# Kernel tuning notes

Measured on AMD Instinct MI355X. Metric: run time of the kernel, lower is better.

The kernel has to match this reference:

```python
import jax, jax.numpy as jnp
import numpy as np

E = 32          # num_experts
K = 4           # num_experts_per_tok
H = 1024        # hidden_size
I = 768         # moe_intermediate_size
ROUTED_SCALING_FACTOR = 1.0


def setup_inputs() -> dict:
    key = jax.random.key(0)
    k0, k1, k2, k3, k4, k5 = jax.random.split(key, 6)
    return {
        "hidden_states": jax.random.normal(k0, (1, 2048, H), jnp.float32),
        "gate_w": jax.random.normal(k1, (E, H), jnp.float32) * 0.02,
        "w1": jax.random.normal(k2, (E, H, I), jnp.float32) * 0.02,   # gate proj per expert
        "w3": jax.random.normal(k3, (E, H, I), jnp.float32) * 0.02,   # up proj per expert
        "w2": jax.random.normal(k4, (E, I, H), jnp.float32) * 0.02,   # down proj per expert
        "e_bias": jax.random.normal(k5, (E,), jnp.float32) * 0.02,    # e_score_correction_bias
    }


def reference(hidden_states, gate_w, w1, w3, w2, e_bias):
    orig_shape = hidden_states.shape
    x = hidden_states.reshape(-1, orig_shape[-1])            # [T, H]
    T = x.shape[0]

    # ----- router gate (ReplicatedLinear, no bias) -----
    router_logits = x @ gate_w.T                             # [T, E]

    # ----- grouped top-k with num_expert_group=1, topk_group=1 == plain top-k
    # scoring_func='sigmoid'; correction bias only affects expert *selection*,
    # the routing weights are the uncorrected sigmoid scores.
    scores = jax.nn.sigmoid(router_logits.astype(jnp.float32))          # [T, E]
    _, topk_ids = jax.lax.top_k(scores + e_bias[None, :], K)            # [T, K]
    topk_w = jnp.take_along_axis(scores, topk_ids, axis=1)              # [T, K]
    # renormalize (norm_topk_prob=True)
    topk_w = topk_w / jnp.sum(topk_w, axis=1, keepdims=True)

    # dense combine weights [T, E] (zero for unselected experts)
    combine = jnp.zeros((T, E), jnp.float32).at[jnp.arange(T)[:, None], topk_ids].add(topk_w)

    # ----- experts: SwiGLU per expert, combine weighted -----
    g = jnp.einsum("th,ehi->tei", x, w1)                     # [T, E, I]
    u = jnp.einsum("th,ehi->tei", x, w3)                     # [T, E, I]
    a = jax.nn.silu(g) * u * combine[:, :, None].astype(x.dtype)
    out = jnp.einsum("tei,eih->th", a, w2)                   # [T, H]

    out = out * ROUTED_SCALING_FACTOR
    return out.reshape(orig_shape)
```

## Files before the change

kernel.cpp:

```cpp
#include <hip/hip_runtime.h>
#include <cstdint>

#define TOK 2048
#define HD  1024
#define ID  768
#define NE  32
#define RT  4

typedef unsigned short u16t;
typedef unsigned int   u32t;
typedef __bf16 bf16x8 __attribute__((ext_vector_type(8)));
typedef float  f32x4  __attribute__((ext_vector_type(4)));
typedef u16t   u16x8  __attribute__((ext_vector_type(8)));
typedef u16t   u16x4  __attribute__((ext_vector_type(4)));
typedef float  fvec4  __attribute__((ext_vector_type(4)));

__device__ __forceinline__ u16t f2b(float f) {
  u32t u = __float_as_uint(f);
  u32t r = u + 0x7fffu + ((u >> 16) & 1u);
  return (u16t)(r >> 16);
}

__device__ __forceinline__ int swz(int row, int kc) {
  return (row * 4 + (kc ^ ((row >> 2) & 3))) * 8;
}

__global__ void k_cvt(const float* __restrict__ x, u16t* __restrict__ xb) {
  int i = (blockIdx.x * 256 + threadIdx.x) * 4;
  fvec4 v = *(const fvec4*)(x + i);
  u16x4 o = { f2b(v[0]), f2b(v[1]), f2b(v[2]), f2b(v[3]) };
  *(u16x4*)(xb + i) = o;
}

__global__ void k_router(const float* __restrict__ x, const float* __restrict__ gw,
                         const float* __restrict__ eb,
                         int* __restrict__ topk_ids, float* __restrict__ topk_w,
                         int* __restrict__ counts) {
  int lane = threadIdx.x & 63;
  int t = blockIdx.x * 4 + (threadIdx.x >> 6);
  const float* xt = x + (size_t)t * HD;
  fvec4 xr[4];
#pragma unroll
  for (int i = 0; i < 4; ++i) xr[i] = *(const fvec4*)(xt + lane * 4 + i * 256);
  float myscore = 0.f;
  for (int e = 0; e < NE; ++e) {
    const float* ge = gw + (size_t)e * HD + lane * 4;
    float s = 0.f;
#pragma unroll
    for (int i = 0; i < 4; ++i) {
      fvec4 g = *(const fvec4*)(ge + i * 256);
      s = fmaf(xr[i][0], g[0], s); s = fmaf(xr[i][1], g[1], s);
      s = fmaf(xr[i][2], g[2], s); s = fmaf(xr[i][3], g[3], s);
    }
#pragma unroll
    for (int off = 32; off; off >>= 1) s += __shfl_xor(s, off);
    if (lane == e) myscore = s;
  }
  float sig = 1.f / (1.f + expf(-myscore));
  float biased = (lane < NE) ? (sig + eb[lane]) : -3.0e38f;
  float wsum = 0.f;
  int ids[4]; float wsv[4];
#pragma unroll
  for (int k = 0; k < 4; ++k) {
    float v = biased; int idx = lane;
#pragma unroll
    for (int off = 32; off; off >>= 1) {
      float ov = __shfl_xor(v, off);
      int   oi = __shfl_xor(idx, off);
      if (ov > v || (ov == v && oi < idx)) { v = ov; idx = oi; }
    }
    ids[k] = idx;
    float sc = __shfl(sig, idx);
    wsv[k] = sc; wsum += sc;
    if (lane == idx) biased = -3.0e38f;
  }
  float inv = 1.f / wsum;
#pragma unroll
  for (int k = 0; k < 4; ++k) {
    if (lane == k) {
      topk_ids[t * 4 + k] = ids[k];
      topk_w[t * 4 + k]  = wsv[k] * inv;
      atomicAdd(&counts[ids[k]], 1);
    }
  }
}

__global__ void k_bucket(const int* __restrict__ topk_ids, const float* __restrict__ topk_w,
                         const int* __restrict__ counts, int* __restrict__ offsets,
                         int* __restrict__ pairTok, float* __restrict__ pairW,
                         int* __restrict__ invp) {
  __shared__ int soff[NE + 1];
  __shared__ int scur[NE];
  int tid = threadIdx.x;
  if (tid == 0) {
    int acc = 0;
    for (int e = 0; e < NE; ++e) { soff[e] = acc; acc += counts[e]; }
    soff[NE] = acc;
  }
  if (tid < NE) scur[tid] = 0;
  __syncthreads();
  if (tid <= NE) offsets[tid] = soff[tid];
  for (int p = tid; p < TOK * 4; p += 256) {
    int e = topk_ids[p];
    int pos = soff[e] + atomicAdd(&scur[e], 1);
    pairTok[pos] = p;
    pairW[pos]   = topk_w[p];
    invp[p]      = pos;
  }
}

__launch_bounds__(256, 2)
__global__ void k_gemm1(const u16t* __restrict__ xb, const float* __restrict__ w1,
                        const float* __restrict__ w3,
                        const int* __restrict__ counts, const int* __restrict__ offsets,
                        const int* __restrict__ pairTok, const float* __restrict__ pairW,
                        u16t* __restrict__ A) {
  const int e = blockIdx.y;
  const int colbase = blockIdx.x * 64;
  const int count = counts[e];
  const int base  = offsets[e];
  const int tid = threadIdx.x, lane = tid & 63, wv = tid >> 6;

  __shared__ __align__(16) u16t Xs[256 * 32];
  __shared__ __align__(16) u16t Ws2[2][64 * 32];
  __shared__ float pw[256];

  const float* wp = (tid < 128) ? (w1 + (size_t)e * HD * ID)
                                : (w3 + (size_t)e * HD * ID);
  u16t* wsp = &Ws2[tid >> 7][0];
  const int u  = tid & 127;
  const int cg = u & 15, hg = u >> 4;
  const int kc = hg >> 1, half = (hg & 1) * 4;

  for (int r0 = blockIdx.z * 256; r0 < count; r0 += RT * 256) {
    __syncthreads();
    int idx = r0 + tid;
    bool valid = idx < count;
    int pr = valid ? (pairTok[base + idx] >> 2) : -1;
    pw[tid] = valid ? pairW[base + idx] : 0.f;

    u16x8 xd[4];
    fvec4 wd[4];
    {
      if (pr >= 0) {
        const u16t* s = xb + (size_t)pr * HD;
        xd[0] = *(const u16x8*)(s);      xd[1] = *(const u16x8*)(s + 8);
        xd[2] = *(const u16x8*)(s + 16); xd[3] = *(const u16x8*)(s + 24);
      } else {
        u16x8 z = {0,0,0,0,0,0,0,0};
        xd[0] = z; xd[1] = z; xd[2] = z; xd[3] = z;
      }
      const float* s = wp + (size_t)(hg * 4) * ID + colbase + cg * 4;
      wd[0] = *(const fvec4*)(s);          wd[1] = *(const fvec4*)(s + ID);
      wd[2] = *(const fvec4*)(s + 2 * ID); wd[3] = *(const fvec4*)(s + 3 * ID);
    }

    f32x4 zz = {0.f, 0.f, 0.f, 0.f};
    f32x4 accg[4][4], accu[4][4];
#pragma unroll
    for (int a = 0; a < 4; ++a)
#pragma unroll
      for (int b = 0; b < 4; ++b) { accg[a][b] = zz; accu[a][b] = zz; }

    for (int kk = 0; kk < HD; kk += 32) {
      __syncthreads();
      *(u16x8*)&Xs[swz(tid, 0)] = xd[0];
      *(u16x8*)&Xs[swz(tid, 1)] = xd[1];
      *(u16x8*)&Xs[swz(tid, 2)] = xd[2];
      *(u16x8*)&Xs[swz(tid, 3)] = xd[3];
#pragma unroll
      for (int c = 0; c < 4; ++c) {
        u16x4 pk = { f2b(wd[0][c]), f2b(wd[1][c]), f2b(wd[2][c]), f2b(wd[3][c]) };
        *(u16x4*)&wsp[swz(cg * 4 + c, kc) + half] = pk;
      }
      __syncthreads();
      if (kk + 32 < HD) {
        if (pr >= 0) {
          const u16t* s = xb + (size_t)pr * HD + kk + 32;
          xd[0] = *(const u16x8*)(s);      xd[1] = *(const u16x8*)(s + 8);
          xd[2] = *(const u16x8*)(s + 16); xd[3] = *(const u16x8*)(s + 24);
        }
        const float* s = wp + (size_t)(kk + 32 + hg * 4) * ID + colbase + cg * 4;
        wd[0] = *(const fvec4*)(s);          wd[1] = *(const fvec4*)(s + ID);
        wd[2] = *(const fvec4*)(s + 2 * ID); wd[3] = *(const fvec4*)(s + 3 * ID);
      }
      const int kcl = lane >> 4;
      const int rb = wv * 64 + (lane & 15);
      bf16x8 af[4];
#pragma unroll
      for (int rf = 0; rf < 4; ++rf)
        af[rf] = *(const bf16x8*)&Xs[swz(rb + rf * 16, kcl)];
#pragma unroll
      for (int cf = 0; cf < 4; ++cf) {
        int col = cf * 16 + (lane & 15);
        bf16x8 b1f = *(const bf16x8*)&Ws2[0][swz(col, kcl)];
        bf16x8 b3f = *(const bf16x8*)&Ws2[1][swz(col, kcl)];
#pragma unroll
        for (int rf = 0; rf < 4; ++rf) {
          accg[rf][cf] = __builtin_amdgcn_mfma_f32_16x16x32_bf16(af[rf], b1f, accg[rf][cf], 0, 0, 0);
          accu[rf][cf] = __builtin_amdgcn_mfma_f32_16x16x32_bf16(af[rf], b3f, accu[rf][cf], 0, 0, 0);
        }
      }
    }
    __syncthreads();
#pragma unroll
    for (int rf = 0; rf < 4; ++rf) {
#pragma unroll
      for (int ri = 0; ri < 4; ++ri) {
        int rowl = wv * 64 + rf * 16 + (lane >> 4) * 4 + ri;
        int grow = r0 + rowl;
        if (grow < count) {
          float wgt = pw[rowl];
#pragma unroll
          for (int cf = 0; cf < 4; ++cf) {
            float gg = accg[rf][cf][ri];
            float uu = accu[rf][cf][ri];
            float a = gg / (1.f + expf(-gg)) * uu * wgt;
            A[(size_t)(base + grow) * ID + colbase + cf * 16 + (lane & 15)] = f2b(a);
          }
        }
      }
    }
  }
}

__launch_bounds__(256, 2)
__global__ void k_gemm2(const u16t* __restrict__ A, const float* __restrict__ w2,
                        const int* __restrict__ counts, const int* __restrict__ offsets,
                        float* __restrict__ buf) {
  const int e = blockIdx.y;
  const int colbase = blockIdx.x * 64;
  const int count = counts[e];
  const int base  = offsets[e];
  const int tid = threadIdx.x, lane = tid & 63, wv = tid >> 6;

  __shared__ __align__(16) u16t As[256 * 32];
  __shared__ __align__(16) u16t W2s[64 * 32];

  const float* w2e = w2 + (size_t)e * ID * HD;
  const int cg = tid & 15, kg = tid >> 4;
  const int k0 = kg * 2, kcw = k0 >> 3, offw = k0 & 7;

  for (int r0 = blockIdx.z * 256; r0 < count; r0 += RT * 256) {
    int idx = r0 + tid;
    bool valid = idx < count;
    const u16t* asrc = A + (size_t)(base + idx) * ID;

    u16x8 xd[4];
    fvec4 wd0, wd1;
    {
      if (valid) {
        xd[0] = *(const u16x8*)(asrc);      xd[1] = *(const u16x8*)(asrc + 8);
        xd[2] = *(const u16x8*)(asrc + 16); xd[3] = *(const u16x8*)(asrc + 24);
      } else {
        u16x8 z = {0,0,0,0,0,0,0,0};
        xd[0] = z; xd[1] = z; xd[2] = z; xd[3] = z;
      }
      const float* s = w2e + (size_t)(kg * 2) * HD + colbase + cg * 4;
      wd0 = *(const fvec4*)(s); wd1 = *(const fvec4*)(s + HD);
    }

    f32x4 zz = {0.f, 0.f, 0.f, 0.f};
    f32x4 acc[4][4];
#pragma unroll
    for (int a = 0; a < 4; ++a)
#pragma unroll
      for (int b = 0; b < 4; ++b) acc[a][b] = zz;

    for (int kk = 0; kk < ID; kk += 32) {
      __syncthreads();
      *(u16x8*)&As[swz(tid, 0)] = xd[0];
      *(u16x8*)&As[swz(tid, 1)] = xd[1];
      *(u16x8*)&As[swz(tid, 2)] = xd[2];
      *(u16x8*)&As[swz(tid, 3)] = xd[3];
#pragma unroll
      for (int c = 0; c < 4; ++c) {
        u32t pk = (u32t)f2b(wd0[c]) | ((u32t)f2b(wd1[c]) << 16);
        *(u32t*)&W2s[swz(cg * 4 + c, kcw) + offw] = pk;
      }
      __syncthreads();
      if (kk + 32 < ID) {
        if (valid) {
          const u16t* s = asrc + kk + 32;
          xd[0] = *(const u16x8*)(s);      xd[1] = *(const u16x8*)(s + 8);
          xd[2] = *(const u16x8*)(s + 16); xd[3] = *(const u16x8*)(s + 24);
        }
        const float* s = w2e + (size_t)(kk + 32 + kg * 2) * HD + colbase + cg * 4;
        wd0 = *(const fvec4*)(s); wd1 = *(const fvec4*)(s + HD);
      }
      const int kcl = lane >> 4;
      const int rb = wv * 64 + (lane & 15);
      bf16x8 af[4];
#pragma unroll
      for (int rf = 0; rf < 4; ++rf)
        af[rf] = *(const bf16x8*)&As[swz(rb + rf * 16, kcl)];
#pragma unroll
      for (int cf = 0; cf < 4; ++cf) {
        bf16x8 bfr = *(const bf16x8*)&W2s[swz(cf * 16 + (lane & 15), kcl)];
#pragma unroll
        for (int rf = 0; rf < 4; ++rf)
          acc[rf][cf] = __builtin_amdgcn_mfma_f32_16x16x32_bf16(af[rf], bfr, acc[rf][cf], 0, 0, 0);
      }
    }
#pragma unroll
    for (int rf = 0; rf < 4; ++rf)
#pragma unroll
      for (int ri = 0; ri < 4; ++ri) {
        int rowl = wv * 64 + rf * 16 + (lane >> 4) * 4 + ri;
        int grow = r0 + rowl;
        if (grow < count) {
#pragma unroll
          for (int cf = 0; cf < 4; ++cf)
            buf[(size_t)(base + grow) * HD + colbase + cf * 16 + (lane & 15)] = acc[rf][cf][ri];
        }
      }
  }
}

__global__ void k_reduce(const float* __restrict__ buf, const int* __restrict__ invp,
                         float* __restrict__ out) {
  int t = blockIdx.x;
  int col = threadIdx.x * 4;
  int p0 = invp[t * 4 + 0], p1 = invp[t * 4 + 1];
  int p2 = invp[t * 4 + 2], p3 = invp[t * 4 + 3];
  fvec4 s = *(const fvec4*)(buf + (size_t)p0 * HD + col);
  s += *(const fvec4*)(buf + (size_t)p1 * HD + col);
  s += *(const fvec4*)(buf + (size_t)p2 * HD + col);
  s += *(const fvec4*)(buf + (size_t)p3 * HD + col);
  *(fvec4*)(out + (size_t)t * HD + col) = s;
}

extern "C" void kernel_launch(void* const* d_in, const int* in_sizes, int n_in,
                              void* d_out, int out_size, void* d_ws, size_t ws_size,
                              hipStream_t stream) {
  const float* x  = (const float*)d_in[0];
  const float* gw = (const float*)d_in[1];
  const float* w1 = (const float*)d_in[2];
  const float* w3 = (const float*)d_in[3];
  const float* w2 = (const float*)d_in[4];
  const float* eb = (const float*)d_in[5];
  float* out = (float*)d_out;

  char* ws = (char*)d_ws;
  int*   counts   = (int*)(ws);
  int*   offsets  = (int*)(ws + 256);
  int*   topk_ids = (int*)(ws + 4096);
  float* topk_w   = (float*)(ws + 36864);
  int*   pairTok  = (int*)(ws + 69632);
  float* pairW    = (float*)(ws + 102400);
  int*   invp     = (int*)(ws + 135168);
  u16t*  xb       = (u16t*)(ws + 262144);
  u16t*  Abuf     = (u16t*)(ws + 262144 + 4194304);
  float* buf      = (float*)(ws + 262144 + 4194304 + 12582912);

  hipMemsetAsync(counts, 0, 4096, stream);
  k_cvt   <<<2048, 256, 0, stream>>>(x, xb);
  k_router<<<512, 256, 0, stream>>>(x, gw, eb, topk_ids, topk_w, counts);
  k_bucket<<<1, 256, 0, stream>>>(topk_ids, topk_w, counts, offsets, pairTok, pairW, invp);
  k_gemm1 <<<dim3(12, 32, RT), 256, 0, stream>>>(xb, w1, w3, counts, offsets, pairTok, pairW, Abuf);
  k_gemm2 <<<dim3(16, 32, RT), 256, 0, stream>>>(Abuf, w2, counts, offsets, buf);
  k_reduce<<<2048, 256, 0, stream>>>(buf, invp, out);
}
```

Before: 241.5 us.

## Double-buffer weight tiles and load activations directly into MFMA fragments

Both expert GEMMs now keep the weight tile in a double-buffered LDS ring and load the activation rows straight from global memory into MFMA A-fragments, so the activation LDS stage goes away. The kernel is software-pipelined two k-steps deep so loads overlap the MFMAs. Column tiles shrink from 64 to 32, the grid widens, RT drops to 2, and launch bounds rise for higher occupancy. In exchange, each activation row is read from global memory by more blocks, and the weight fp32-to-bf16 conversion is repeated across more row blocks.

```diff
diff --git a/kernel.cpp b/kernel.cpp
--- a/kernel.cpp
+++ b/kernel.cpp
@@ -5,7 +5,7 @@
 #define HD  1024
 #define ID  768
 #define NE  32
-#define RT  4
+#define RT  2
 
 typedef unsigned short u16t;
 typedef unsigned int   u32t;
@@ -109,102 +109,98 @@
   }
 }
 
-__launch_bounds__(256, 2)
+#define G1_WLOAD(d0, d1, KK) do { \
+    const float* _s = wp + (size_t)((KK) + hg * 2) * ID + wcol; \
+    d0 = *(const fvec4*)(_s); d1 = *(const fvec4*)(_s + ID); } while (0)
+
+#define G1_WSTORE(BUF, d0, d1) do { \
+    _Pragma("unroll") for (int c = 0; c < 4; ++c) { \
+      u32t pk = (u32t)f2b(d0[c]) | ((u32t)f2b(d1[c]) << 16); \
+      *(u32t*)&Ws[BUF][mat][swz(cg4 + c, kcw) + offw] = pk; } } while (0)
+
+#define G1_AFLOAD(AF, KK) do { \
+    _Pragma("unroll") for (int rf = 0; rf < 4; ++rf) \
+      AF[rf] = *(const u16x8*)(xb + (size_t)tok[rf] * HD + (KK) + klo); } while (0)
+
+#define G1_MFMA(AF, BUF) do { \
+    bf16x8 b0 = *(const bf16x8*)&Ws[BUF][0][swz(col0, kcl)]; \
+    bf16x8 b1 = *(const bf16x8*)&Ws[BUF][0][swz(col1, kcl)]; \
+    bf16x8 b2 = *(const bf16x8*)&Ws[BUF][1][swz(col0, kcl)]; \
+    bf16x8 b3 = *(const bf16x8*)&Ws[BUF][1][swz(col1, kcl)]; \
+    _Pragma("unroll") for (int rf = 0; rf < 4; ++rf) { \
+      acc[rf][0][0] = __builtin_amdgcn_mfma_f32_16x16x32_bf16(AF[rf], b0, acc[rf][0][0], 0, 0, 0); \
+      acc[rf][1][0] = __builtin_amdgcn_mfma_f32_16x16x32_bf16(AF[rf], b1, acc[rf][1][0], 0, 0, 0); \
+      acc[rf][0][1] = __builtin_amdgcn_mfma_f32_16x16x32_bf16(AF[rf], b2, acc[rf][0][1], 0, 0, 0); \
+      acc[rf][1][1] = __builtin_amdgcn_mfma_f32_16x16x32_bf16(AF[rf], b3, acc[rf][1][1], 0, 0, 0); } } while (0)
+
+__launch_bounds__(256, 3)
 __global__ void k_gemm1(const u16t* __restrict__ xb, const float* __restrict__ w1,
                         const float* __restrict__ w3,
                         const int* __restrict__ counts, const int* __restrict__ offsets,
                         const int* __restrict__ pairTok, const float* __restrict__ pairW,
                         u16t* __restrict__ A) {
   const int e = blockIdx.y;
-  const int colbase = blockIdx.x * 64;
+  const int colbase = blockIdx.x * 32;
   const int count = counts[e];
   const int base  = offsets[e];
   const int tid = threadIdx.x, lane = tid & 63, wv = tid >> 6;
 
-  __shared__ __align__(16) u16t Xs[256 * 32];
-  __shared__ __align__(16) u16t Ws2[2][64 * 32];
+  __shared__ __align__(16) u16t Ws[2][2][1024];
   __shared__ float pw[256];
 
-  const float* wp = (tid < 128) ? (w1 + (size_t)e * HD * ID)
-                                : (w3 + (size_t)e * HD * ID);
-  u16t* wsp = &Ws2[tid >> 7][0];
-  const int u  = tid & 127;
-  const int cg = u & 15, hg = u >> 4;
-  const int kc = hg >> 1, half = (hg & 1) * 4;
+  const int mat = tid >> 7;
+  const float* wp = (mat ? w3 : w1) + (size_t)e * HD * ID;
+  const int u = tid & 127;
+  const int cg4 = (u & 7) * 4, hg = u >> 3;
+  const int kcw = hg >> 2, offw = (hg & 3) * 2;
+  const int wcol = colbase + cg4;
+  const int klo = (lane >> 4) * 8;
+  const int col0 = lane & 15, col1 = col0 + 16, kcl = lane >> 4;
 
   for (int r0 = blockIdx.z * 256; r0 < count; r0 += RT * 256) {
     __syncthreads();
-    int idx = r0 + tid;
-    bool valid = idx < count;
-    int pr = valid ? (pairTok[base + idx] >> 2) : -1;
-    pw[tid] = valid ? pairW[base + idx] : 0.f;
-
-    u16x8 xd[4];
-    fvec4 wd[4];
     {
-      if (pr >= 0) {
-        const u16t* s = xb + (size_t)pr * HD;
-        xd[0] = *(const u16x8*)(s);      xd[1] = *(const u16x8*)(s + 8);
-        xd[2] = *(const u16x8*)(s + 16); xd[3] = *(const u16x8*)(s + 24);
-      } else {
-        u16x8 z = {0,0,0,0,0,0,0,0};
-        xd[0] = z; xd[1] = z; xd[2] = z; xd[3] = z;
-      }
-      const float* s = wp + (size_t)(hg * 4) * ID + colbase + cg * 4;
-      wd[0] = *(const fvec4*)(s);          wd[1] = *(const fvec4*)(s + ID);
-      wd[2] = *(const fvec4*)(s + 2 * ID); wd[3] = *(const fvec4*)(s + 3 * ID);
+      int idx = r0 + tid;
+      pw[tid] = (idx < count) ? pairW[base + idx] : 0.f;
+    }
+    int tok[4];
+#pragma unroll
+    for (int rf = 0; rf < 4; ++rf) {
+      int idx = r0 + wv * 64 + rf * 16 + (lane & 15);
+      idx = idx < count ? idx : count - 1;
+      tok[rf] = pairTok[base + idx] >> 2;
     }
 
     f32x4 zz = {0.f, 0.f, 0.f, 0.f};
-    f32x4 accg[4][4], accu[4][4];
+    f32x4 acc[4][2][2];
 #pragma unroll
     for (int a = 0; a < 4; ++a)
 #pragma unroll
-      for (int b = 0; b < 4; ++b) { accg[a][b] = zz; accu[a][b] = zz; }
-
-    for (int kk = 0; kk < HD; kk += 32) {
+      for (int b = 0; b < 2; ++b) { acc[a][b][0] = zz; acc[a][b][1] = zz; }
+
+    fvec4 wdA0, wdA1, wdB0, wdB1;
+    u16x8 afC[4], afD[4];
+    G1_WLOAD(wdA0, wdA1, 0);
+    G1_WLOAD(wdB0, wdB1, 32);
+    G1_AFLOAD(afC, 0);
+    G1_WSTORE(0, wdA0, wdA1);
+    G1_WLOAD(wdA0, wdA1, 64);
+
+    for (int s = 0; s < 32; s += 2) {
+      const int kk = s * 32;
       __syncthreads();
-      *(u16x8*)&Xs[swz(tid, 0)] = xd[0];
-      *(u16x8*)&Xs[swz(tid, 1)] = xd[1];
-      *(u16x8*)&Xs[swz(tid, 2)] = xd[2];
-      *(u16x8*)&Xs[swz(tid, 3)] = xd[3];
-#pragma unroll
-      for (int c = 0; c < 4; ++c) {
-        u16x4 pk = { f2b(wd[0][c]), f2b(wd[1][c]), f2b(wd[2][c]), f2b(wd[3][c]) };
-        *(u16x4*)&wsp[swz(cg * 4 + c, kc) + half] = pk;
-      }
+      G1_WSTORE(1, wdB0, wdB1);
+      if (s + 3 < 32) G1_WLOAD(wdB0, wdB1, kk + 96);
+      G1_AFLOAD(afD, kk + 32);
+      G1_MFMA(afC, 0);
       __syncthreads();
-      if (kk + 32 < HD) {
-        if (pr >= 0) {
-          const u16t* s = xb + (size_t)pr * HD + kk + 32;
-          xd[0] = *(const u16x8*)(s);      xd[1] = *(const u16x8*)(s + 8);
-          xd[2] = *(const u16x8*)(s + 16); xd[3] = *(const u16x8*)(s + 24);
-        }
-        const float* s = wp + (size_t)(kk + 32 + hg * 4) * ID + colbase + cg * 4;
-        wd[0] = *(const fvec4*)(s);          wd[1] = *(const fvec4*)(s + ID);
-        wd[2] = *(const fvec4*)(s + 2 * ID); wd[3] = *(const fvec4*)(s + 3 * ID);
-      }
-      const int kcl = lane >> 4;
-      const int rb = wv * 64 + (lane & 15);
-      bf16x8 af[4];
-#pragma unroll
-      for (int rf = 0; rf < 4; ++rf)
-        af[rf] = *(const bf16x8*)&Xs[swz(rb + rf * 16, kcl)];
-#pragma unroll
-      for (int cf = 0; cf < 4; ++cf) {
-        int col = cf * 16 + (lane & 15);
-        bf16x8 b1f = *(const bf16x8*)&Ws2[0][swz(col, kcl)];
-        bf16x8 b3f = *(const bf16x8*)&Ws2[1][swz(col, kcl)];
-#pragma unroll
-        for (int rf = 0; rf < 4; ++rf) {
-          accg[rf][cf] = __builtin_amdgcn_mfma_f32_16x16x32_bf16(af[rf], b1f, accg[rf][cf], 0, 0, 0);
-          accu[rf][cf] = __builtin_amdgcn_mfma_f32_16x16x32_bf16(af[rf], b3f, accu[rf][cf], 0, 0, 0);
-        }
-      }
-    }
-    __syncthreads();
-#pragma unroll
-    for (int rf = 0; rf < 4; ++rf) {
+      if (s + 2 < 32) G1_WSTORE(0, wdA0, wdA1);
+      if (s + 4 < 32) G1_WLOAD(wdA0, wdA1, kk + 128);
+      if (s + 2 < 32) G1_AFLOAD(afC, kk + 64);
+      G1_MFMA(afD, 1);
+    }
+#pragma unroll
+    for (int rf = 0; rf < 4; ++rf)
 #pragma unroll
       for (int ri = 0; ri < 4; ++ri) {
         int rowl = wv * 64 + rf * 16 + (lane >> 4) * 4 + ri;
@@ -212,95 +208,87 @@
         if (grow < count) {
           float wgt = pw[rowl];
 #pragma unroll
-          for (int cf = 0; cf < 4; ++cf) {
-            float gg = accg[rf][cf][ri];
-            float uu = accu[rf][cf][ri];
+          for (int cf = 0; cf < 2; ++cf) {
+            float gg = acc[rf][cf][0][ri];
+            float uu = acc[rf][cf][1][ri];
             float a = gg / (1.f + expf(-gg)) * uu * wgt;
             A[(size_t)(base + grow) * ID + colbase + cf * 16 + (lane & 15)] = f2b(a);
           }
         }
       }
-    }
-  }
-}
-
-__launch_bounds__(256, 2)
-__global__ void k_gemm2(const u16t* __restrict__ A, const float* __restrict__ w2,
+  }
+}
+
+#define G2_WLOAD(d, KK) \
+    d = *(const fvec4*)(w2e + (size_t)((KK) + kg) * HD + wcol)
+
+#define G2_WSTORE(BUF, d) do { \
+    _Pragma("unroll") for (int c = 0; c < 4; ++c) \
+      W2s[BUF][swz(cg4 + c, kcw) + offw] = f2b(d[c]); } while (0)
+
+#define G2_AFLOAD(AF, KK) do { \
+    _Pragma("unroll") for (int rf = 0; rf < 4; ++rf) \
+      AF[rf] = *(const u16x8*)(Ab + (size_t)arow[rf] * ID + (KK) + klo); } while (0)
+
+#define G2_MFMA(AF, BUF) do { \
+    bf16x8 b0 = *(const bf16x8*)&W2s[BUF][swz(col0, kcl)]; \
+    bf16x8 b1 = *(const bf16x8*)&W2s[BUF][swz(col1, kcl)]; \
+    _Pragma("unroll") for (int rf = 0; rf < 4; ++rf) { \
+      acc[rf][0] = __builtin_amdgcn_mfma_f32_16x16x32_bf16(AF[rf], b0, acc[rf][0], 0, 0, 0); \
+      acc[rf][1] = __builtin_amdgcn_mfma_f32_16x16x32_bf16(AF[rf], b1, acc[rf][1], 0, 0, 0); } } while (0)
+
+__launch_bounds__(256, 4)
+__global__ void k_gemm2(const u16t* __restrict__ Ab, const float* __restrict__ w2,
                         const int* __restrict__ counts, const int* __restrict__ offsets,
                         float* __restrict__ buf) {
   const int e = blockIdx.y;
-  const int colbase = blockIdx.x * 64;
+  const int colbase = blockIdx.x * 32;
   const int count = counts[e];
   const int base  = offsets[e];
   const int tid = threadIdx.x, lane = tid & 63, wv = tid >> 6;
 
-  __shared__ __align__(16) u16t As[256 * 32];
-  __shared__ __align__(16) u16t W2s[64 * 32];
+  __shared__ __align__(16) u16t W2s[2][1024];
 
   const float* w2e = w2 + (size_t)e * ID * HD;
-  const int cg = tid & 15, kg = tid >> 4;
-  const int k0 = kg * 2, kcw = k0 >> 3, offw = k0 & 7;
+  const int cg4 = (tid & 7) * 4, kg = tid >> 3;
+  const int kcw = kg >> 3, offw = kg & 7;
+  const int wcol = colbase + cg4;
+  const int klo = (lane >> 4) * 8;
+  const int col0 = lane & 15, col1 = col0 + 16, kcl = lane >> 4;
 
   for (int r0 = blockIdx.z * 256; r0 < count; r0 += RT * 256) {
-    int idx = r0 + tid;
-    bool valid = idx < count;
-    const u16t* asrc = A + (size_t)(base + idx) * ID;
-
-    u16x8 xd[4];
-    fvec4 wd0, wd1;
-    {
-      if (valid) {
-        xd[0] = *(const u16x8*)(asrc);      xd[1] = *(const u16x8*)(asrc + 8);
-        xd[2] = *(const u16x8*)(asrc + 16); xd[3] = *(const u16x8*)(asrc + 24);
-      } else {
-        u16x8 z = {0,0,0,0,0,0,0,0};
-        xd[0] = z; xd[1] = z; xd[2] = z; xd[3] = z;
-      }
-      const float* s = w2e + (size_t)(kg * 2) * HD + colbase + cg * 4;
-      wd0 = *(const fvec4*)(s); wd1 = *(const fvec4*)(s + HD);
-    }
-
+    int arow[4];
+#pragma unroll
+    for (int rf = 0; rf < 4; ++rf) {
+      int idx = r0 + wv * 64 + rf * 16 + (lane & 15);
+      idx = idx < count ? idx : count - 1;
+      arow[rf] = base + idx;
+    }
     f32x4 zz = {0.f, 0.f, 0.f, 0.f};
-    f32x4 acc[4][4];
-#pragma unroll
-    for (int a = 0; a < 4; ++a)
-#pragma unroll
-      for (int b = 0; b < 4; ++b) acc[a][b] = zz;
-
-    for (int kk = 0; kk < ID; kk += 32) {
+    f32x4 acc[4][2];
+#pragma unroll
+    for (int a = 0; a < 4; ++a) { acc[a][0] = zz; acc[a][1] = zz; }
+
+    fvec4 wdA, wdB;
+    u16x8 afC[4], afD[4];
+    G2_WLOAD(wdA, 0);
+    G2_WLOAD(wdB, 32);
+    G2_AFLOAD(afC, 0);
+    G2_WSTORE(0, wdA);
+    G2_WLOAD(wdA, 64);
+
+    for (int s = 0; s < 24; s += 2) {
+      const int kk = s * 32;
       __syncthreads();
-      *(u16x8*)&As[swz(tid, 0)] = xd[0];
-      *(u16x8*)&As[swz(tid, 1)] = xd[1];
-      *(u16x8*)&As[swz(tid, 2)] = xd[2];
-      *(u16x8*)&As[swz(tid, 3)] = xd[3];
-#pragma unroll
-      for (int c = 0; c < 4; ++c) {
-        u32t pk = (u32t)f2b(wd0[c]) | ((u32t)f2b(wd1[c]) << 16);
-        *(u32t*)&W2s[swz(cg * 4 + c, kcw) + offw] = pk;
-      }
+      G2_WSTORE(1, wdB);
+      if (s + 3 < 24) G2_WLOAD(wdB, kk + 96);
+      G2_AFLOAD(afD, kk + 32);
+      G2_MFMA(afC, 0);
       __syncthreads();
-      if (kk + 32 < ID) {
-        if (valid) {
-          const u16t* s = asrc + kk + 32;
-          xd[0] = *(const u16x8*)(s);      xd[1] = *(const u16x8*)(s + 8);
-          xd[2] = *(const u16x8*)(s + 16); xd[3] = *(const u16x8*)(s + 24);
-        }
-        const float* s = w2e + (size_t)(kk + 32 + kg * 2) * HD + colbase + cg * 4;
-        wd0 = *(const fvec4*)(s); wd1 = *(const fvec4*)(s + HD);
-      }
-      const int kcl = lane >> 4;
-      const int rb = wv * 64 + (lane & 15);
-      bf16x8 af[4];
-#pragma unroll
-      for (int rf = 0; rf < 4; ++rf)
-        af[rf] = *(const bf16x8*)&As[swz(rb + rf * 16, kcl)];
-#pragma unroll
-      for (int cf = 0; cf < 4; ++cf) {
-        bf16x8 bfr = *(const bf16x8*)&W2s[swz(cf * 16 + (lane & 15), kcl)];
-#pragma unroll
-        for (int rf = 0; rf < 4; ++rf)
-          acc[rf][cf] = __builtin_amdgcn_mfma_f32_16x16x32_bf16(af[rf], bfr, acc[rf][cf], 0, 0, 0);
-      }
+      if (s + 2 < 24) G2_WSTORE(0, wdA);
+      if (s + 4 < 24) G2_WLOAD(wdA, kk + 128);
+      if (s + 2 < 24) G2_AFLOAD(afC, kk + 64);
+      G2_MFMA(afD, 1);
     }
 #pragma unroll
     for (int rf = 0; rf < 4; ++rf)
@@ -310,10 +298,11 @@
         int grow = r0 + rowl;
         if (grow < count) {
 #pragma unroll
-          for (int cf = 0; cf < 4; ++cf)
+          for (int cf = 0; cf < 2; ++cf)
             buf[(size_t)(base + grow) * HD + colbase + cf * 16 + (lane & 15)] = acc[rf][cf][ri];
         }
       }
+    __syncthreads();
   }
 }
 
@@ -357,7 +346,7 @@
   k_cvt   <<<2048, 256, 0, stream>>>(x, xb);
   k_router<<<512, 256, 0, stream>>>(x, gw, eb, topk_ids, topk_w, counts);
   k_bucket<<<1, 256, 0, stream>>>(topk_ids, topk_w, counts, offsets, pairTok, pairW, invp);
-  k_gemm1 <<<dim3(12, 32, RT), 256, 0, stream>>>(xb, w1, w3, counts, offsets, pairTok, pairW, Abuf);
-  k_gemm2 <<<dim3(16, 32, RT), 256, 0, stream>>>(Abuf, w2, counts, offsets, buf);
+  k_gemm1 <<<dim3(24, 32, RT), 256, 0, stream>>>(xb, w1, w3, counts, offsets, pairTok, pairW, Abuf);
+  k_gemm2 <<<dim3(32, 32, RT), 256, 0, stream>>>(Abuf, w2, counts, offsets, buf);
   k_reduce<<<2048, 256, 0, stream>>>(buf, invp, out);
 }
```

Result: slower. 299.2 us (+23.9%).
